# Optimization experiments

Measured on AMD Instinct MI355X. Metric: run time of the kernel, lower is better.

## Reference

```python
import jax, jax.numpy as jnp
import numpy as np

B, N, E, D, H, M = 64, 4096, 8192, 256, 256, 64


def setup_inputs() -> dict:
    key = jax.random.key(0)
    ks = jax.random.split(key, 12)
    s = lambda fan_in: 1.0 / np.sqrt(fan_in)
    return {
        "node_embeddings": jax.random.normal(ks[0], (B, N, D), jnp.float32),
        "army_counts": jax.random.randint(ks[1], (B, N), 0, 50).astype(jnp.float32),
        "action_edges": jax.random.randint(ks[2], (B, E, 2), 0, N, dtype=jnp.int32),
        # edge_scorer: Linear(2H, H) -> ReLU -> Linear(H, 1)
        "W1": jax.random.normal(ks[3], (2 * H, H), jnp.float32) * s(2 * H),
        "b1": jnp.zeros((H,), jnp.float32),
        "W2": jax.random.normal(ks[4], (H, 1), jnp.float32) * s(H),
        "b2": jnp.zeros((1,), jnp.float32),
        # army_scorer: Linear(2D, 128) -> ReLU -> Linear(128, M)
        "A1": jax.random.normal(ks[5], (2 * D, 128), jnp.float32) * s(2 * D),
        "a1": jnp.zeros((128,), jnp.float32),
        "A2": jax.random.normal(ks[6], (128, M), jnp.float32) * s(128.0),
        "a2": jnp.zeros((M,), jnp.float32),
    }


def reference(node_embeddings, army_counts, W1, b1, W2, b2, A1, a1, A2, a2, action_edges):
    # node_embeddings: [B, N, D]; action_edges: [B, E, 2]; army_counts: [B, N]
    b, n, d = node_embeddings.shape
    m = A2.shape[1]
    dt = node_embeddings.dtype

    src = action_edges[..., 0]  # [B, E]
    tgt = action_edges[..., 1]
    src_c = jnp.clip(src, 0, n - 1)
    tgt_c = jnp.clip(tgt, 0, n - 1)

    # Gather endpoint embeddings: [B, E, D]
    src_e = jnp.take_along_axis(node_embeddings, src_c[..., None], axis=1)
    tgt_e = jnp.take_along_axis(node_embeddings, tgt_c[..., None], axis=1)
    edge_embed = jnp.concatenate([src_e, tgt_e], axis=-1)  # [B, E, 2D]

    # edge scorer MLP -> [B, E]
    h = jax.nn.relu(edge_embed @ W1 + b1)
    edge_logits = (h @ W2 + b2)[..., 0]

    # army scorer MLP -> [B, E, M]
    g = jax.nn.relu(edge_embed @ A1 + a1)
    army_logits = g @ A2 + a2

    src_armies = jnp.take_along_axis(army_counts, src_c, axis=1)  # [B, E]
    tgt_armies = jnp.take_along_axis(army_counts, tgt_c, axis=1)

    valid_edges = (src >= 0) & (tgt >= 0)
    bad_edges = valid_edges & ((src_armies <= 2) | (tgt_armies >= 3 * src_armies))
    edge_logits = edge_logits - bad_edges.astype(dt) * 1.0

    invalid_self = (src == tgt) & valid_edges
    edge_logits = edge_logits - invalid_self.astype(dt) * 100.0

    max_sendable = src_armies - 1  # [B, E]
    army_range = jnp.arange(m, dtype=dt)[None, None, :]  # [1, 1, M]
    valid_mask = army_range <= max_sendable[..., None]
    army_logits = jnp.where(valid_mask, army_logits, jnp.asarray(-1e9, dt))

    return edge_logits, army_logits
```

## Files before the change

### kernel.cpp

```cpp
#include <hip/hip_runtime.h>

#define BB   64
#define NN   4096
#define EE   8192
#define DD   256
#define HH   256
#define MM   64
#define K1   512
#define NC   384
#define TE   64
#define BLOCK 512
#define KC   64
#define NCHUNK 8
#define ASTR 88
#define GSTR 136
#define ABUF (64 * ASTR)
#define SMEM_SHORTS (2 * ABUF)
#define BE_TOT (BB * EE)
#define WCTF_ELEMS (NC * K1)
#define A2F_ELEMS  (128 * MM)
#define WS_NEEDED ((size_t)(WCTF_ELEMS + A2F_ELEMS) * sizeof(short))

typedef float f32x4 __attribute__((ext_vector_type(4)));
typedef short bf16x8 __attribute__((ext_vector_type(8)));

__device__ __forceinline__ short f2bf(float f) {
    unsigned u = __float_as_uint(f);
    unsigned r = (u + 0x7fffu + ((u >> 16) & 1u)) >> 16;
    return (short)r;
}

__device__ __forceinline__ int cvt_pk_bf16(float lo, float hi) {
    int r;
    asm("v_cvt_pk_bf16_f32 %0, %1, %2" : "=v"(r) : "v"(lo), "v"(hi));
    return r;
}

__device__ __forceinline__ void barrier_lgkm() {
    asm volatile("s_waitcnt lgkmcnt(0)\n\ts_barrier" ::: "memory");
}

__global__ void AttackHead_prep(const float* __restrict__ W1,
                                const float* __restrict__ A1,
                                const float* __restrict__ A2,
                                short* __restrict__ wctf,
                                short* __restrict__ a2f) {
    int t = blockIdx.x * 256 + threadIdx.x;
    if (t < 131072) {
        int k = t >> 8, n = t & 255;
        int c = k >> 5, kr = k & 31, quad = kr >> 3, j = kr & 7;
        int nt = n >> 4, l15 = n & 15;
        wctf[((c * 24 + nt) * 64 + quad * 16 + l15) * 8 + j] = f2bf(W1[t]);
    } else if (t < 131072 + 65536) {
        int t2 = t - 131072;
        int k = t2 >> 7, n = 256 + (t2 & 127);
        int c = k >> 5, kr = k & 31, quad = kr >> 3, j = kr & 7;
        int nt = n >> 4, l15 = n & 15;
        wctf[((c * 24 + nt) * 64 + quad * 16 + l15) * 8 + j] = f2bf(A1[t2]);
    } else if (t < 131072 + 65536 + 8192) {
        int t3 = t - 131072 - 65536;
        int k = t3 >> 6, n = t3 & 63;
        int ks = k >> 5, kr = k & 31, quad = kr >> 3, j = kr & 7;
        int nt2 = n >> 4, l15 = n & 15;
        a2f[((ks * 4 + nt2) * 64 + quad * 16 + l15) * 8 + j] = f2bf(A2[t3]);
    }
}

template <bool USE_WS>
__device__ __forceinline__ bf16x8 load_bfrag(const short* __restrict__ wf,
                                             const float* __restrict__ W1,
                                             const float* __restrict__ A1,
                                             int c, int nt, int lane) {
    if (USE_WS) {
        return *(const bf16x8*)(wf + ((c * 24 + nt) * 64 + lane) * 8);
    } else {
        int l15 = lane & 15, quad = lane >> 4;
        int n = nt * 16 + l15;
        bf16x8 r;
        #pragma unroll
        for (int j = 0; j < 8; ++j) {
            int k = c * 32 + quad * 8 + j;
            float v = (n < HH) ? W1[k * HH + n] : A1[k * 128 + (n - HH)];
            r[j] = f2bf(v);
        }
        return r;
    }
}

template <bool USE_WS>
__device__ __forceinline__ bf16x8 load_a2frag(const short* __restrict__ a2f,
                                              const float* __restrict__ A2,
                                              int ks, int nt2, int lane) {
    if (USE_WS) {
        return *(const bf16x8*)(a2f + ((ks * 4 + nt2) * 64 + lane) * 8);
    } else {
        int l15 = lane & 15, quad = lane >> 4;
        int n = nt2 * 16 + l15;
        bf16x8 r;
        #pragma unroll
        for (int j = 0; j < 8; ++j) {
            int k = ks * 32 + quad * 8 + j;
            r[j] = f2bf(A2[k * MM + n]);
        }
        return r;
    }
}

template <bool USE_WS>
__global__ __launch_bounds__(BLOCK, 4)
void AttackHead_main(const float* __restrict__ nodes,
                     const float* __restrict__ army,
                     const int* __restrict__ edges,
                     const float* __restrict__ W1,
                     const float* __restrict__ b1,
                     const float* __restrict__ W2,
                     const float* __restrict__ b2,
                     const float* __restrict__ A1,
                     const float* __restrict__ a1,
                     const float* __restrict__ A2,
                     const float* __restrict__ a2,
                     const short* __restrict__ wctf,
                     const short* __restrict__ a2f,
                     float* __restrict__ out) {
    __shared__ __align__(16) short smem[SMEM_SHORTS];
    __shared__ int   srcn[TE], tgtn[TE];
    __shared__ float elog[TE], maxs[TE];

    const int tid = threadIdx.x;
    const int bb  = ((blockIdx.x & 7) << 10) | (blockIdx.x >> 3);
    const int bglob = bb >> 7;
    const long be0 = (long)bb * TE;

    if (tid < TE) {
        long be = be0 + tid;
        int src = edges[2 * be], tgt = edges[2 * be + 1];
        int sc = min(max(src, 0), NN - 1);
        int tc = min(max(tgt, 0), NN - 1);
        srcn[tid] = sc; tgtn[tid] = tc;
        float sa = army[(size_t)bglob * NN + sc];
        float ta = army[(size_t)bglob * NN + tc];
        bool valid = (src >= 0) && (tgt >= 0);
        bool bad   = valid && (sa <= 2.0f || ta >= 3.0f * sa);
        bool selfe = valid && (src == tgt);
        elog[tid] = b2[0] - (bad ? 1.0f : 0.0f) - (selfe ? 100.0f : 0.0f);
        maxs[tid] = sa - 1.0f;
    }

    const int w    = tid >> 6;
    const int lane = tid & 63;
    const int quad = lane >> 4;
    const int l15  = lane & 15;

    bf16x8 bfc0 = load_bfrag<USE_WS>(wctf, W1, A1, 0, w * 3 + 0, lane);
    bf16x8 bfc1 = load_bfrag<USE_WS>(wctf, W1, A1, 0, w * 3 + 1, lane);
    bf16x8 bfc2 = load_bfrag<USE_WS>(wctf, W1, A1, 0, w * 3 + 2, lane);

    __syncthreads();

    const int srow = tid >> 3;
    const int sj   = tid & 7;
    const size_t nbase_g = (size_t)bglob * NN;
    const float* srcp = nodes + (nbase_g + (size_t)srcn[srow]) * DD + sj * 8;
    const float* tgtp = nodes + (nbase_g + (size_t)tgtn[srow]) * DD + sj * 8;

    f32x4 acc[4][3] = {};

    {
        float4 v0 = *(const float4*)(srcp);
        float4 v1 = *(const float4*)(srcp + 4);
        int4 s;
        s.x = cvt_pk_bf16(v0.x, v0.y); s.y = cvt_pk_bf16(v0.z, v0.w);
        s.z = cvt_pk_bf16(v1.x, v1.y); s.w = cvt_pk_bf16(v1.z, v1.w);
        *(int4*)(&smem[srow * ASTR + sj * 8]) = s;
    }
    float4 lda0 = *(const float4*)(srcp + 64);
    float4 lda1 = *(const float4*)(srcp + 68);

    #pragma unroll
    for (int c = 0; c < NCHUNK; ++c) {
        barrier_lgkm();

        float4 ldn0, ldn1;
        if (c + 2 < NCHUNK) {
            const float* p = ((c + 2) < 4 ? srcp : tgtp) + ((c + 2) & 3) * 64;
            ldn0 = *(const float4*)(p);
            ldn1 = *(const float4*)(p + 4);
        }

        bf16x8 bg0 = load_bfrag<USE_WS>(wctf, W1, A1, 2 * c + 1, w * 3 + 0, lane);
        bf16x8 bg1 = load_bfrag<USE_WS>(wctf, W1, A1, 2 * c + 1, w * 3 + 1, lane);
        bf16x8 bg2 = load_bfrag<USE_WS>(wctf, W1, A1, 2 * c + 1, w * 3 + 2, lane);

        const short* Ab = &smem[(c & 1) * ABUF];

        bf16x8 af[4];
        #pragma unroll
        for (int mt = 0; mt < 4; ++mt)
            af[mt] = *(const bf16x8*)(&Ab[(mt * 16 + l15) * ASTR + quad * 8]);
        #pragma unroll
        for (int mt = 0; mt < 4; ++mt) {
            acc[mt][0] = __builtin_amdgcn_mfma_f32_16x16x32_bf16(af[mt], bfc0, acc[mt][0], 0, 0, 0);
            acc[mt][1] = __builtin_amdgcn_mfma_f32_16x16x32_bf16(af[mt], bfc1, acc[mt][1], 0, 0, 0);
            acc[mt][2] = __builtin_amdgcn_mfma_f32_16x16x32_bf16(af[mt], bfc2, acc[mt][2], 0, 0, 0);
        }

        if (c + 1 < NCHUNK) {
            bfc0 = load_bfrag<USE_WS>(wctf, W1, A1, 2 * c + 2, w * 3 + 0, lane);
            bfc1 = load_bfrag<USE_WS>(wctf, W1, A1, 2 * c + 2, w * 3 + 1, lane);
            bfc2 = load_bfrag<USE_WS>(wctf, W1, A1, 2 * c + 2, w * 3 + 2, lane);
        }

        bf16x8 ag[4];
        #pragma unroll
        for (int mt = 0; mt < 4; ++mt)
            ag[mt] = *(const bf16x8*)(&Ab[(mt * 16 + l15) * ASTR + 32 + quad * 8]);
        #pragma unroll
        for (int mt = 0; mt < 4; ++mt) {
            acc[mt][0] = __builtin_amdgcn_mfma_f32_16x16x32_bf16(ag[mt], bg0, acc[mt][0], 0, 0, 0);
            acc[mt][1] = __builtin_amdgcn_mfma_f32_16x16x32_bf16(ag[mt], bg1, acc[mt][1], 0, 0, 0);
            acc[mt][2] = __builtin_amdgcn_mfma_f32_16x16x32_bf16(ag[mt], bg2, acc[mt][2], 0, 0, 0);
        }

        if (c + 1 < NCHUNK) {
            int4 s;
            s.x = cvt_pk_bf16(lda0.x, lda0.y); s.y = cvt_pk_bf16(lda0.z, lda0.w);
            s.z = cvt_pk_bf16(lda1.x, lda1.y); s.w = cvt_pk_bf16(lda1.z, lda1.w);
            *(int4*)(&smem[((c + 1) & 1) * ABUF + srow * ASTR + sj * 8]) = s;
        }
        if (c + 2 < NCHUNK) { lda0 = ldn0; lda1 = ldn1; }
    }

    __syncthreads();

    short* Gs = smem;
    float ep[4][4] = {};
    #pragma unroll
    for (int jn = 0; jn < 3; ++jn) {
        int ct = (w * 3 + jn) * 16 + l15;
        float bias = (ct < HH) ? b1[ct] : a1[ct - HH];
        if (ct < HH) {
            float w2v = W2[ct];
            #pragma unroll
            for (int mt = 0; mt < 4; ++mt)
                #pragma unroll
                for (int r = 0; r < 4; ++r) {
                    float h = fmaxf(acc[mt][jn][r] + bias, 0.0f);
                    ep[mt][r] += h * w2v;
                }
        } else {
            int gc = ct - HH;
            #pragma unroll
            for (int mt = 0; mt < 4; ++mt)
                #pragma unroll
                for (int r = 0; r < 4; ++r) {
                    float g = fmaxf(acc[mt][jn][r] + bias, 0.0f);
                    Gs[(mt * 16 + quad * 4 + r) * GSTR + gc] = f2bf(g);
                }
        }
    }
    if (w < 6) {
        #pragma unroll
        for (int msk = 1; msk <= 8; msk <<= 1)
            #pragma unroll
            for (int mt = 0; mt < 4; ++mt)
                #pragma unroll
                for (int r = 0; r < 4; ++r)
                    ep[mt][r] += __shfl_xor(ep[mt][r], msk, 64);
        if (l15 == 0) {
            #pragma unroll
            for (int mt = 0; mt < 4; ++mt)
                #pragma unroll
                for (int r = 0; r < 4; ++r)
                    atomicAdd(&elog[mt * 16 + quad * 4 + r], ep[mt][r]);
        }
    }
    __syncthreads();

    const int mt2 = w >> 1;
    const int nh  = w & 1;
    f32x4 acc2[2] = {};
    #pragma unroll
    for (int ks = 0; ks < 4; ++ks) {
        bf16x8 ga = *(const bf16x8*)(&Gs[(mt2 * 16 + l15) * GSTR + ks * 32 + quad * 8]);
        #pragma unroll
        for (int nb = 0; nb < 2; ++nb) {
            bf16x8 bv = load_a2frag<USE_WS>(a2f, A2, ks, nh * 2 + nb, lane);
            acc2[nb] = __builtin_amdgcn_mfma_f32_16x16x32_bf16(ga, bv, acc2[nb], 0, 0, 0);
        }
    }

    if (tid < TE) out[be0 + tid] = elog[tid];

    #pragma unroll
    for (int nb = 0; nb < 2; ++nb) {
        int col = (nh * 2 + nb) * 16 + l15;
        float a2v = a2[col];
        #pragma unroll
        for (int r = 0; r < 4; ++r) {
            int grow = mt2 * 16 + quad * 4 + r;
            float val = acc2[nb][r] + a2v;
            if ((float)col > maxs[grow]) val = -1e9f;
            out[(size_t)BE_TOT + (size_t)(be0 + grow) * MM + col] = val;
        }
    }
}

extern "C" void kernel_launch(void* const* d_in, const int* in_sizes, int n_in,
                              void* d_out, int out_size, void* d_ws, size_t ws_size,
                              hipStream_t stream) {
    const float* nodes = (const float*)d_in[0];
    const float* army  = (const float*)d_in[1];
    const int*   edges = (const int*)d_in[2];
    const float* W1    = (const float*)d_in[3];
    const float* b1    = (const float*)d_in[4];
    const float* W2    = (const float*)d_in[5];
    const float* b2    = (const float*)d_in[6];
    const float* A1    = (const float*)d_in[7];
    const float* a1    = (const float*)d_in[8];
    const float* A2    = (const float*)d_in[9];
    const float* a2    = (const float*)d_in[10];
    float* out = (float*)d_out;

    int nblocks = BE_TOT / TE;

    if (ws_size >= WS_NEEDED) {
        short* wctf = (short*)d_ws;
        short* a2f  = wctf + WCTF_ELEMS;
        AttackHead_prep<<<800, 256, 0, stream>>>(W1, A1, A2, wctf, a2f);
        AttackHead_main<true><<<nblocks, BLOCK, 0, stream>>>(
            nodes, army, edges, W1, b1, W2, b2, A1, a1, A2, a2, wctf, a2f, out);
    } else {
        AttackHead_main<false><<<nblocks, BLOCK, 0, stream>>>(
            nodes, army, edges, W1, b1, W2, b2, A1, a1, A2, a2,
            (const short*)nullptr, (const short*)nullptr, out);
    }
}
```

Measured before the change: 642.4 us.

## Precompute per-node first-layer projections, then combine per edge

Splits the first layer of both MLPs into source and target halves and multiplies every node embedding by them once, in a new bf16 MFMA GEMM kernel. The results go to a large workspace buffer. A second kernel gathers the two endpoint rows for each edge, adds them with the bias and applies ReLU, then finishes the edge-score dot product and the small army GEMM. This replaces per-edge K=512 GEMMs with per-node K=256 GEMMs, roughly halving the MFMA work. In exchange it writes and then randomly re-reads a workspace of about 512 MB, and it stores the edge-scorer hidden values in bf16.

```diff
diff --git a/kernel.cpp b/kernel.cpp
--- a/kernel.cpp
+++ b/kernel.cpp
@@ -19,7 +19,10 @@
 #define BE_TOT (BB * EE)
 #define WCTF_ELEMS (NC * K1)
 #define A2F_ELEMS  (128 * MM)
-#define WS_NEEDED ((size_t)(WCTF_ELEMS + A2F_ELEMS) * sizeof(short))
+#define WS_FRAG ((size_t)(WCTF_ELEMS + A2F_ELEMS) * sizeof(short))
+#define PRE_ROW 2048
+#define WS_PRE ((size_t)BB * NN * PRE_ROW)
+#define WS_BIG (WS_FRAG + WS_PRE)
 
 typedef float f32x4 __attribute__((ext_vector_type(4)));
 typedef short bf16x8 __attribute__((ext_vector_type(8)));
@@ -29,16 +32,18 @@
     unsigned r = (u + 0x7fffu + ((u >> 16) & 1u)) >> 16;
     return (short)r;
 }
-
+__device__ __forceinline__ float bf2f(short s) {
+    return __uint_as_float(((unsigned)(unsigned short)s) << 16);
+}
 __device__ __forceinline__ int cvt_pk_bf16(float lo, float hi) {
     int r;
     asm("v_cvt_pk_bf16_f32 %0, %1, %2" : "=v"(r) : "v"(lo), "v"(hi));
     return r;
 }
-
 __device__ __forceinline__ void barrier_lgkm() {
     asm volatile("s_waitcnt lgkmcnt(0)\n\ts_barrier" ::: "memory");
 }
+
 
 __global__ void AttackHead_prep(const float* __restrict__ W1,
                                 const float* __restrict__ A1,
@@ -305,6 +310,251 @@
     }
 }
 
+
+__global__ void AttackHead_prep2(const float* __restrict__ W1,
+                                 const float* __restrict__ A1,
+                                 const float* __restrict__ A2,
+                                 short* __restrict__ wctf2,
+                                 short* __restrict__ a2f) {
+    int t = blockIdx.x * 256 + threadIdx.x;
+    if (t < 196608) {
+        int k = t / 768, n = t - k * 768;
+        float v;
+        if (n < 256)       v = W1[k * 256 + n];
+        else if (n < 512)  v = W1[(256 + k) * 256 + (n - 256)];
+        else if (n < 640)  v = A1[k * 128 + (n - 512)];
+        else               v = A1[(256 + k) * 128 + (n - 640)];
+        int c = k >> 5, kr = k & 31, quad = kr >> 3, j = kr & 7;
+        int nt = n >> 4, l15 = n & 15;
+        wctf2[((c * 48 + nt) * 64 + quad * 16 + l15) * 8 + j] = f2bf(v);
+    } else if (t < 196608 + 8192) {
+        int t3 = t - 196608;
+        int k = t3 >> 6, n = t3 & 63;
+        int ks = k >> 5, kr = k & 31, quad = kr >> 3, j = kr & 7;
+        int nt2 = n >> 4, l15 = n & 15;
+        a2f[((ks * 4 + nt2) * 64 + quad * 16 + l15) * 8 + j] = f2bf(A2[t3]);
+    }
+}
+
+__global__ __launch_bounds__(512, 4)
+void AttackHead_pregemm(const float* __restrict__ nodes,
+                        const short* __restrict__ wctf2,
+                        char* __restrict__ pre) {
+    __shared__ __align__(16) short smem[SMEM_SHORTS];
+    const int tid = threadIdx.x;
+    const int bb = ((blockIdx.x & 7) << 10) | (blockIdx.x >> 3);
+    const int rowgrp = bb >> 1;
+    const int nhalf  = bb & 1;
+
+    const int w    = tid >> 6;
+    const int lane = tid & 63;
+    const int quad = lane >> 4;
+    const int l15  = lane & 15;
+    const int srow = tid >> 3;
+    const int sj   = tid & 7;
+
+    const float* Arowp = nodes + ((size_t)rowgrp * 64 + srow) * 256 + sj * 8;
+    const int ntb = nhalf * 24 + w * 3;
+
+    bf16x8 bfc0 = *(const bf16x8*)(wctf2 + ((0 * 48 + ntb + 0) * 64 + lane) * 8);
+    bf16x8 bfc1 = *(const bf16x8*)(wctf2 + ((0 * 48 + ntb + 1) * 64 + lane) * 8);
+    bf16x8 bfc2 = *(const bf16x8*)(wctf2 + ((0 * 48 + ntb + 2) * 64 + lane) * 8);
+
+    f32x4 acc[4][3] = {};
+
+    {
+        float4 v0 = *(const float4*)(Arowp);
+        float4 v1 = *(const float4*)(Arowp + 4);
+        int4 s;
+        s.x = cvt_pk_bf16(v0.x, v0.y); s.y = cvt_pk_bf16(v0.z, v0.w);
+        s.z = cvt_pk_bf16(v1.x, v1.y); s.w = cvt_pk_bf16(v1.z, v1.w);
+        *(int4*)(&smem[srow * ASTR + sj * 8]) = s;
+    }
+    float4 lda0 = *(const float4*)(Arowp + 64);
+    float4 lda1 = *(const float4*)(Arowp + 68);
+
+    #pragma unroll
+    for (int c = 0; c < 4; ++c) {
+        barrier_lgkm();
+
+        float4 ldn0, ldn1;
+        if (c + 2 < 4) {
+            const float* p = Arowp + (c + 2) * 64;
+            ldn0 = *(const float4*)(p);
+            ldn1 = *(const float4*)(p + 4);
+        }
+
+        bf16x8 bg0 = *(const bf16x8*)(wctf2 + (((2 * c + 1) * 48 + ntb + 0) * 64 + lane) * 8);
+        bf16x8 bg1 = *(const bf16x8*)(wctf2 + (((2 * c + 1) * 48 + ntb + 1) * 64 + lane) * 8);
+        bf16x8 bg2 = *(const bf16x8*)(wctf2 + (((2 * c + 1) * 48 + ntb + 2) * 64 + lane) * 8);
+
+        const short* Ab = &smem[(c & 1) * ABUF];
+
+        bf16x8 af[4];
+        #pragma unroll
+        for (int mt = 0; mt < 4; ++mt)
+            af[mt] = *(const bf16x8*)(&Ab[(mt * 16 + l15) * ASTR + quad * 8]);
+        #pragma unroll
+        for (int mt = 0; mt < 4; ++mt) {
+            acc[mt][0] = __builtin_amdgcn_mfma_f32_16x16x32_bf16(af[mt], bfc0, acc[mt][0], 0, 0, 0);
+            acc[mt][1] = __builtin_amdgcn_mfma_f32_16x16x32_bf16(af[mt], bfc1, acc[mt][1], 0, 0, 0);
+            acc[mt][2] = __builtin_amdgcn_mfma_f32_16x16x32_bf16(af[mt], bfc2, acc[mt][2], 0, 0, 0);
+        }
+
+        if (c + 1 < 4) {
+            bfc0 = *(const bf16x8*)(wctf2 + (((2 * c + 2) * 48 + ntb + 0) * 64 + lane) * 8);
+            bfc1 = *(const bf16x8*)(wctf2 + (((2 * c + 2) * 48 + ntb + 1) * 64 + lane) * 8);
+            bfc2 = *(const bf16x8*)(wctf2 + (((2 * c + 2) * 48 + ntb + 2) * 64 + lane) * 8);
+        }
+
+        bf16x8 ag[4];
+        #pragma unroll
+        for (int mt = 0; mt < 4; ++mt)
+            ag[mt] = *(const bf16x8*)(&Ab[(mt * 16 + l15) * ASTR + 32 + quad * 8]);
+        #pragma unroll
+        for (int mt = 0; mt < 4; ++mt) {
+            acc[mt][0] = __builtin_amdgcn_mfma_f32_16x16x32_bf16(ag[mt], bg0, acc[mt][0], 0, 0, 0);
+            acc[mt][1] = __builtin_amdgcn_mfma_f32_16x16x32_bf16(ag[mt], bg1, acc[mt][1], 0, 0, 0);
+            acc[mt][2] = __builtin_amdgcn_mfma_f32_16x16x32_bf16(ag[mt], bg2, acc[mt][2], 0, 0, 0);
+        }
+
+        if (c + 1 < 4) {
+            int4 s;
+            s.x = cvt_pk_bf16(lda0.x, lda0.y); s.y = cvt_pk_bf16(lda0.z, lda0.w);
+            s.z = cvt_pk_bf16(lda1.x, lda1.y); s.w = cvt_pk_bf16(lda1.z, lda1.w);
+            *(int4*)(&smem[((c + 1) & 1) * ABUF + srow * ASTR + sj * 8]) = s;
+        }
+        if (c + 2 < 4) { lda0 = ldn0; lda1 = ldn1; }
+    }
+
+    char* rowbase = pre + (size_t)rowgrp * 64 * PRE_ROW;
+    #pragma unroll
+    for (int jn = 0; jn < 3; ++jn) {
+        int col = (ntb + jn) * 16 + l15;
+        if (col < 512) {
+            #pragma unroll
+            for (int mt = 0; mt < 4; ++mt)
+                #pragma unroll
+                for (int r = 0; r < 4; ++r) {
+                    int row = mt * 16 + quad * 4 + r;
+                    *(short*)(rowbase + (size_t)row * PRE_ROW + 2 * col) = f2bf(acc[mt][jn][r]);
+                }
+        } else {
+            #pragma unroll
+            for (int mt = 0; mt < 4; ++mt)
+                #pragma unroll
+                for (int r = 0; r < 4; ++r) {
+                    int row = mt * 16 + quad * 4 + r;
+                    *(float*)(rowbase + (size_t)row * PRE_ROW + 1024 + 4 * (col - 512)) = acc[mt][jn][r];
+                }
+        }
+    }
+}
+
+__global__ __launch_bounds__(256, 8)
+void AttackHead_edge(const char* __restrict__ pre,
+                     const float* __restrict__ army,
+                     const int* __restrict__ edges,
+                     const float* __restrict__ b1,
+                     const float* __restrict__ W2,
+                     const float* __restrict__ b2,
+                     const float* __restrict__ a1,
+                     const short* __restrict__ a2f,
+                     const float* __restrict__ a2,
+                     float* __restrict__ out) {
+    __shared__ __align__(16) short Gs[TE * GSTR];
+    __shared__ int   srcn[TE], tgtn[TE];
+    __shared__ float elog[TE], maxs[TE];
+    __shared__ float b1s[256], W2s[256], a1s[128];
+
+    const int tid = threadIdx.x;
+    const int bb  = ((blockIdx.x & 7) << 10) | (blockIdx.x >> 3);
+    const int bglob = bb >> 7;
+    const long be0 = (long)bb * TE;
+
+    if (tid < TE) {
+        long be = be0 + tid;
+        int src = edges[2 * be], tgt = edges[2 * be + 1];
+        int sc = min(max(src, 0), NN - 1);
+        int tc = min(max(tgt, 0), NN - 1);
+        srcn[tid] = sc; tgtn[tid] = tc;
+        float sa = army[(size_t)bglob * NN + sc];
+        float ta = army[(size_t)bglob * NN + tc];
+        bool valid = (src >= 0) && (tgt >= 0);
+        bool bad   = valid && (sa <= 2.0f || ta >= 3.0f * sa);
+        bool selfe = valid && (src == tgt);
+        elog[tid] = b2[0] - (bad ? 1.0f : 0.0f) - (selfe ? 100.0f : 0.0f);
+        maxs[tid] = sa - 1.0f;
+    }
+    b1s[tid] = b1[tid];
+    W2s[tid] = W2[tid];
+    if (tid < 128) a1s[tid] = a1[tid];
+    __syncthreads();
+
+    const int e = tid & 63;
+    const int j = tid >> 6;
+    const char* sp = pre + (size_t)((size_t)bglob * NN + srcn[e]) * PRE_ROW;
+    const char* tp = pre + (size_t)((size_t)bglob * NN + tgtn[e]) * PRE_ROW;
+
+    float dot = 0.0f;
+    #pragma unroll
+    for (int b = 0; b < 8; ++b) {
+        bf16x8 hs = *(const bf16x8*)(sp + j * 128 + b * 16);
+        bf16x8 ht = *(const bf16x8*)(tp + 512 + j * 128 + b * 16);
+        #pragma unroll
+        for (int i = 0; i < 8; ++i) {
+            int col = j * 64 + b * 8 + i;
+            float h = fmaxf(bf2f(hs[i]) + bf2f(ht[i]) + b1s[col], 0.0f);
+            dot = fmaf(h, W2s[col], dot);
+        }
+    }
+    #pragma unroll
+    for (int b = 0; b < 8; ++b) {
+        float4 gs = *(const float4*)(sp + 1024 + j * 128 + b * 16);
+        float4 gt = *(const float4*)(tp + 1536 + j * 128 + b * 16);
+        int gc = j * 32 + b * 4;
+        float g0 = fmaxf(gs.x + gt.x + a1s[gc + 0], 0.0f);
+        float g1 = fmaxf(gs.y + gt.y + a1s[gc + 1], 0.0f);
+        float g2 = fmaxf(gs.z + gt.z + a1s[gc + 2], 0.0f);
+        float g3 = fmaxf(gs.w + gt.w + a1s[gc + 3], 0.0f);
+        int2 pk;
+        pk.x = cvt_pk_bf16(g0, g1);
+        pk.y = cvt_pk_bf16(g2, g3);
+        *(int2*)(&Gs[e * GSTR + gc]) = pk;
+    }
+    atomicAdd(&elog[e], dot);
+    __syncthreads();
+
+    const int lane = tid & 63;
+    const int quad = lane >> 4;
+    const int l15  = lane & 15;
+    f32x4 acc2[4] = {};
+    #pragma unroll
+    for (int ks = 0; ks < 4; ++ks) {
+        bf16x8 ga = *(const bf16x8*)(&Gs[(j * 16 + l15) * GSTR + ks * 32 + quad * 8]);
+        #pragma unroll
+        for (int nt2 = 0; nt2 < 4; ++nt2) {
+            bf16x8 bv = *(const bf16x8*)(a2f + ((ks * 4 + nt2) * 64 + lane) * 8);
+            acc2[nt2] = __builtin_amdgcn_mfma_f32_16x16x32_bf16(ga, bv, acc2[nt2], 0, 0, 0);
+        }
+    }
+
+    if (tid < TE) out[be0 + tid] = elog[tid];
+
+    #pragma unroll
+    for (int nt2 = 0; nt2 < 4; ++nt2) {
+        int col = nt2 * 16 + l15;
+        float a2v = a2[col];
+        #pragma unroll
+        for (int r = 0; r < 4; ++r) {
+            int grow = j * 16 + quad * 4 + r;
+            float val = acc2[nt2][r] + a2v;
+            if ((float)col > maxs[grow]) val = -1e9f;
+            out[(size_t)BE_TOT + (size_t)(be0 + grow) * MM + col] = val;
+        }
+    }
+}
+
 extern "C" void kernel_launch(void* const* d_in, const int* in_sizes, int n_in,
                               void* d_out, int out_size, void* d_ws, size_t ws_size,
                               hipStream_t stream) {
@@ -323,12 +573,20 @@
 
     int nblocks = BE_TOT / TE;
 
-    if (ws_size >= WS_NEEDED) {
+    if (ws_size >= WS_BIG) {
+        short* wctf2 = (short*)d_ws;
+        short* a2fp  = wctf2 + WCTF_ELEMS;
+        char*  pre   = (char*)d_ws + WS_FRAG;
+        AttackHead_prep2<<<800, 256, 0, stream>>>(W1, A1, A2, wctf2, a2fp);
+        AttackHead_pregemm<<<8192, 512, 0, stream>>>(nodes, wctf2, pre);
+        AttackHead_edge<<<8192, 256, 0, stream>>>(pre, army, edges, b1, W2, b2,
+                                                  a1, a2fp, a2, out);
+    } else if (ws_size >= WS_FRAG) {
         short* wctf = (short*)d_ws;
-        short* a2f  = wctf + WCTF_ELEMS;
-        AttackHead_prep<<<800, 256, 0, stream>>>(W1, A1, A2, wctf, a2f);
+        short* a2fp = wctf + WCTF_ELEMS;
+        AttackHead_prep<<<800, 256, 0, stream>>>(W1, A1, A2, wctf, a2fp);
         AttackHead_main<true><<<nblocks, BLOCK, 0, stream>>>(
-            nodes, army, edges, W1, b1, W2, b2, A1, a1, A2, a2, wctf, a2f, out);
+            nodes, army, edges, W1, b1, W2, b2, A1, a1, A2, a2, wctf, a2fp, out);
     } else {
         AttackHead_main<false><<<nblocks, BLOCK, 0, stream>>>(
             nodes, army, edges, W1, b1, W2, b2, A1, a1, A2, a2,
```

New measurement: 921.3 us. +43.4%, slower.
